# Kernel tuning notes

Hardware: AMD Instinct MI355X
Metric: run time of the kernel (lower is better)

Reference implementation:

```python
import jax, jax.numpy as jnp
import numpy as np

N_NODES = 100000


def _gcn_norm(edge_index, n):
    # add self-loops, then symmetric deg^{-1/2} normalization (PyG GCNConv default)
    loop = jnp.arange(n, dtype=edge_index.dtype)
    src = jnp.concatenate([edge_index[0], loop])
    dst = jnp.concatenate([edge_index[1], loop])
    ones = jnp.ones(src.shape[0], dtype=jnp.float32)
    deg = jax.ops.segment_sum(ones, dst, num_segments=n)
    dinv = jnp.where(deg > 0, jax.lax.rsqrt(deg), 0.0)
    norm = dinv[src] * dinv[dst]  # [E + N]
    return src, dst, norm


def _gcn_conv(x, src, dst, norm, W, b, n):
    h = x @ W                                    # [N, out] transform first (out <= in)
    msg = norm[:, None] * h[src]                 # [E+N, out]
    agg = jax.ops.segment_sum(msg, dst, num_segments=n)
    return agg + b


def reference(x, edge_index, W1, b1, W2, b2):
    n = x.shape[0]
    src, dst, norm = _gcn_norm(edge_index, n)
    h = jax.nn.relu(_gcn_conv(x, src, dst, norm, W1, b1, n))
    # dropout is identity in eval mode (training=False)
    h = jax.nn.relu(_gcn_conv(h, src, dst, norm, W2, b2, n))
    return jax.nn.log_softmax(h, axis=1)


def setup_inputs() -> dict:
    key = jax.random.key(0)
    k1, k2, k3, k4 = jax.random.split(key, 4)
    n, e, f, h, c = N_NODES, 1600000, 500, 64, 40
    x = jax.random.normal(k1, (n, f), dtype=jnp.float32)
    edge_index = jax.random.randint(k2, (2, e), 0, n, dtype=jnp.int64)
    W1 = jax.random.normal(k3, (f, h), dtype=jnp.float32) * (1.0 / np.sqrt(f))
    b1 = jnp.zeros((h,), dtype=jnp.float32)
    W2 = jax.random.normal(k4, (h, c), dtype=jnp.float32) * (1.0 / np.sqrt(h))
    b2 = jnp.zeros((c,), dtype=jnp.float32)
    return {"x": x, "edge_index": edge_index, "W1": W1, "b1": b1, "W2": W2, "b2": b2}
```

## Files before the change

kernel.cpp:

```cpp
#include <hip/hip_runtime.h>

#define NN_F 500
#define HID 64
#define NC 40
#define SCAN_T 256
#define SCAN_E 8
#define SCAN_B (SCAN_T * SCAN_E)
#define LDS_S 40

typedef short s8v __attribute__((ext_vector_type(8)));
typedef short s4v __attribute__((ext_vector_type(4)));
typedef float f4v __attribute__((ext_vector_type(4)));

__device__ __forceinline__ unsigned short rne_bf16(float x) {
    unsigned u = __float_as_uint(x);
    return (unsigned short)((u + 0x7fffu + ((u >> 16) & 1u)) >> 16);
}
__device__ __forceinline__ float bf16_lo(unsigned v) {
    return __uint_as_float(v << 16);
}
__device__ __forceinline__ float bf16_hi(unsigned v) {
    return __uint_as_float(v & 0xffff0000u);
}

__device__ __forceinline__ int load_edge(const void* ei, long long idx, int is64) {
    if (is64) return (int)((const long long*)ei)[idx];
    return ((const int*)ei)[idx];
}

__global__ __launch_bounds__(256) void detect_kernel(const unsigned int* w, int* flag) {
    __shared__ unsigned int red[256];
    unsigned int acc = 0;
    for (int i = threadIdx.x; i < 2048; i += 256) acc |= w[2 * i + 1];
    red[threadIdx.x] = acc;
    __syncthreads();
    for (int s = 128; s > 0; s >>= 1) {
        if (threadIdx.x < s) red[threadIdx.x] |= red[threadIdx.x + s];
        __syncthreads();
    }
    if (threadIdx.x == 0) flag[0] = (red[0] == 0u) ? 1 : 0;
}

__global__ __launch_bounds__(256) void deg_kernel(const void* ei, const int* flag,
                                                  int* deg, int E) {
    int is64 = flag[0];
    long long e = (long long)blockIdx.x * 256 + threadIdx.x;
    if (e < E) {
        int d = load_edge(ei, (long long)E + e, is64);
        atomicAdd(&deg[d], 1);
    }
}

__global__ __launch_bounds__(SCAN_T) void scan1(const int* __restrict__ deg,
                                                int* __restrict__ off,
                                                int* __restrict__ bsums,
                                                float* __restrict__ dinv, int n) {
    __shared__ int lds[SCAN_T];
    int base = blockIdx.x * SCAN_B + threadIdx.x * SCAN_E;
    int v[SCAN_E];
    int local = 0;
#pragma unroll
    for (int k = 0; k < SCAN_E; ++k) {
        int i = base + k;
        v[k] = (i < n) ? deg[i] : 0;
        if (i < n) dinv[i] = rsqrtf((float)v[k] + 1.0f);
        local += v[k];
    }
    lds[threadIdx.x] = local;
    __syncthreads();
    for (int o = 1; o < SCAN_T; o <<= 1) {
        int t = (threadIdx.x >= o) ? lds[threadIdx.x - o] : 0;
        __syncthreads();
        lds[threadIdx.x] += t;
        __syncthreads();
    }
    int prefix = lds[threadIdx.x] - local;
    if (threadIdx.x == SCAN_T - 1) bsums[blockIdx.x] = lds[threadIdx.x];
    int run = prefix;
#pragma unroll
    for (int k = 0; k < SCAN_E; ++k) {
        if (base + k < n) { off[base + k] = run; run += v[k]; }
    }
}

__global__ void scan2(int* bsums, int* off, int nb, int n) {
    int lane = threadIdx.x;
    if (nb <= 64) {
        int v = (lane < nb) ? bsums[lane] : 0;
        int incl = v;
#pragma unroll
        for (int o = 1; o < 64; o <<= 1) {
            int t = __shfl_up(incl, o);
            if (lane >= o) incl += t;
        }
        if (lane < nb) bsums[lane] = incl - v;
        if (lane == 63) off[n] = incl;
    } else if (lane == 0) {
        int run = 0;
        for (int i = 0; i < nb; ++i) { int t = bsums[i]; bsums[i] = run; run += t; }
        off[n] = run;
    }
}

__global__ __launch_bounds__(SCAN_T) void scan3(int* __restrict__ off,
                                                int* __restrict__ cur,
                                                const int* __restrict__ bsums, int n) {
    int base = blockIdx.x * SCAN_B + threadIdx.x * SCAN_E;
    int add = bsums[blockIdx.x];
#pragma unroll
    for (int k = 0; k < SCAN_E; ++k) {
        int i = base + k;
        if (i < n) { int v = off[i] + add; off[i] = v; cur[i] = v; }
    }
}

__global__ __launch_bounds__(256) void build_kernel(const void* ei, const int* flag,
                                                    const float* __restrict__ dinv,
                                                    int* __restrict__ cur,
                                                    int2* __restrict__ csr, int E) {
    int is64 = flag[0];
    long long e = (long long)blockIdx.x * 256 + threadIdx.x;
    if (e >= E) return;
    int s = load_edge(ei, e, is64);
    int d = load_edge(ei, (long long)E + e, is64);
    int pos = atomicAdd(&cur[d], 1);
    csr[pos] = make_int2(s, (int)__float_as_uint(dinv[s] * dinv[d]));
}

__global__ __launch_bounds__(256) void wprep2(const float* __restrict__ W1,
                                              const float* __restrict__ W2,
                                              unsigned short* __restrict__ Wt1,
                                              unsigned short* __restrict__ Wt2) {
    int id = blockIdx.x * 256 + threadIdx.x;
    if (id < 64 * 512) {
        int nn = id >> 9, k = id & 511;
        float v = (k < NN_F) ? W1[k * HID + nn] : 0.f;
        Wt1[id] = rne_bf16(v);
    } else {
        int id2 = id - 64 * 512;
        if (id2 >= 64 * 64) return;
        int nn = id2 >> 6, k = id2 & 63;
        float v = (nn < NC) ? W2[k * NC + nn] : 0.f;
        Wt2[id2] = rne_bf16(v);
    }
}

template<int KPAD>
__global__ __launch_bounds__(256) void gemm_mfma(const float* __restrict__ A,
                                                 const unsigned short* __restrict__ Wh,
                                                 unsigned short* __restrict__ out,
                                                 int n, int K) {
    __shared__ unsigned short Xh[128 * LDS_S];
    __shared__ unsigned short Bh[64 * LDS_S];
    const int t = threadIdx.x;
    const int row0 = blockIdx.x * 128;
    const int wid = t >> 6, lane = t & 63, q = lane >> 4, nn = lane & 15;

    f4v acc[2][4];
#pragma unroll
    for (int mt = 0; mt < 2; ++mt)
#pragma unroll
        for (int ct = 0; ct < 4; ++ct) acc[mt][ct] = (f4v){0.f, 0.f, 0.f, 0.f};

    for (int k0 = 0; k0 < KPAD; k0 += 32) {
        {
            int bn = t >> 2, kq = t & 3;
            *(s8v*)&Bh[bn * LDS_S + kq * 8] = *(const s8v*)&Wh[bn * KPAD + k0 + kq * 8];
        }
        {
            int kq = t & 7, rbase = t >> 3;
#pragma unroll
            for (int rr = 0; rr < 4; ++rr) {
                int row = rr * 32 + rbase;
                int grow = row0 + row;
                int k = k0 + kq * 4;
                float v0 = 0.f, v1 = 0.f, v2 = 0.f, v3 = 0.f;
                if (grow < n) {
                    if (k + 4 <= K) {
                        float4 v = *(const float4*)&A[(long long)grow * K + k];
                        v0 = v.x; v1 = v.y; v2 = v.z; v3 = v.w;
                    } else {
                        if (k + 0 < K) v0 = A[(long long)grow * K + k + 0];
                        if (k + 1 < K) v1 = A[(long long)grow * K + k + 1];
                        if (k + 2 < K) v2 = A[(long long)grow * K + k + 2];
                        if (k + 3 < K) v3 = A[(long long)grow * K + k + 3];
                    }
                }
                s4v h4;
                h4[0] = (short)rne_bf16(v0);
                h4[1] = (short)rne_bf16(v1);
                h4[2] = (short)rne_bf16(v2);
                h4[3] = (short)rne_bf16(v3);
                *(s4v*)&Xh[row * LDS_S + kq * 4] = h4;
            }
        }
        __syncthreads();

        const s8v ah0 = *(const s8v*)&Xh[(wid * 32 + nn) * LDS_S + q * 8];
        const s8v ah1 = *(const s8v*)&Xh[(wid * 32 + 16 + nn) * LDS_S + q * 8];
#pragma unroll
        for (int ct = 0; ct < 4; ++ct) {
            const s8v bh = *(const s8v*)&Bh[(ct * 16 + nn) * LDS_S + q * 8];
            acc[0][ct] = __builtin_amdgcn_mfma_f32_16x16x32_bf16(ah0, bh, acc[0][ct], 0, 0, 0);
            acc[1][ct] = __builtin_amdgcn_mfma_f32_16x16x32_bf16(ah1, bh, acc[1][ct], 0, 0, 0);
        }
        __syncthreads();
    }

#pragma unroll
    for (int mt = 0; mt < 2; ++mt)
#pragma unroll
        for (int ct = 0; ct < 4; ++ct)
#pragma unroll
            for (int r = 0; r < 4; ++r) {
                int row = row0 + wid * 32 + mt * 16 + q * 4 + r;
                if (row < n) out[(long long)row * 64 + ct * 16 + nn] = rne_bf16(acc[mt][ct][r]);
            }
}

#define FMA8(W, H)                                          \
    acc[0] = fmaf(W, bf16_lo((H).x), acc[0]);               \
    acc[1] = fmaf(W, bf16_hi((H).x), acc[1]);               \
    acc[2] = fmaf(W, bf16_lo((H).y), acc[2]);               \
    acc[3] = fmaf(W, bf16_hi((H).y), acc[3]);               \
    acc[4] = fmaf(W, bf16_lo((H).z), acc[4]);               \
    acc[5] = fmaf(W, bf16_hi((H).z), acc[5]);               \
    acc[6] = fmaf(W, bf16_lo((H).w), acc[6]);               \
    acc[7] = fmaf(W, bf16_hi((H).w), acc[7])

__global__ __launch_bounds__(256) void gather_l1(const int2* __restrict__ csr,
                                                 const int* __restrict__ off,
                                                 const unsigned short* __restrict__ h,
                                                 const float* __restrict__ dinv,
                                                 const float* __restrict__ b,
                                                 float* __restrict__ agg, int n) {
    const int lane = threadIdx.x & 63;
    const int g = lane >> 3, fl = lane & 7;
    const int node = __builtin_amdgcn_readfirstlane(blockIdx.x * 4 + (threadIdx.x >> 6));
    if (node >= n) return;
    const int start = off[node], end = off[node + 1];
    float acc[8];
#pragma unroll
    for (int k = 0; k < 8; ++k) acc[k] = 0.f;
    int j = start;
    for (; j + 16 <= end; j += 16) {
        int2 ea = csr[j + g];
        int2 eb = csr[j + 8 + g];
        uint4 ha = *(const uint4*)(h + (long long)ea.x * 64 + fl * 8);
        uint4 hb = *(const uint4*)(h + (long long)eb.x * 64 + fl * 8);
        float wa = __uint_as_float((unsigned)ea.y);
        float wb = __uint_as_float((unsigned)eb.y);
        FMA8(wa, ha);
        FMA8(wb, hb);
    }
    for (; j < end; j += 8) {
        int jj = j + g;
        int2 e = csr[jj < end ? jj : end - 1];
        float w = (jj < end) ? __uint_as_float((unsigned)e.y) : 0.f;
        uint4 hv = *(const uint4*)(h + (long long)e.x * 64 + fl * 8);
        FMA8(w, hv);
    }
#pragma unroll
    for (int k = 0; k < 8; ++k) {
        acc[k] += __shfl_xor(acc[k], 8);
        acc[k] += __shfl_xor(acc[k], 16);
        acc[k] += __shfl_xor(acc[k], 32);
    }
    if (g == 0) {
        float dv = dinv[node];
        float w = dv * dv;
        uint4 hn = *(const uint4*)(h + (long long)node * 64 + fl * 8);
        FMA8(w, hn);
        float4 b4a = ((const float4*)b)[fl * 2];
        float4 b4b = ((const float4*)b)[fl * 2 + 1];
        float4 o0, o1;
        o0.x = acc[0] + b4a.x; o0.x = o0.x > 0.f ? o0.x : 0.f;
        o0.y = acc[1] + b4a.y; o0.y = o0.y > 0.f ? o0.y : 0.f;
        o0.z = acc[2] + b4a.z; o0.z = o0.z > 0.f ? o0.z : 0.f;
        o0.w = acc[3] + b4a.w; o0.w = o0.w > 0.f ? o0.w : 0.f;
        o1.x = acc[4] + b4b.x; o1.x = o1.x > 0.f ? o1.x : 0.f;
        o1.y = acc[5] + b4b.y; o1.y = o1.y > 0.f ? o1.y : 0.f;
        o1.z = acc[6] + b4b.z; o1.z = o1.z > 0.f ? o1.z : 0.f;
        o1.w = acc[7] + b4b.w; o1.w = o1.w > 0.f ? o1.w : 0.f;
        float4* dst = (float4*)(agg + (long long)node * 64 + fl * 8);
        dst[0] = o0;
        dst[1] = o1;
    }
}

__global__ __launch_bounds__(256) void gather_l2(const int2* __restrict__ csr,
                                                 const int* __restrict__ off,
                                                 const unsigned short* __restrict__ h,
                                                 const float* __restrict__ dinv,
                                                 const float* __restrict__ b,
                                                 float* __restrict__ out, int n) {
    const int lane = threadIdx.x & 63;
    const int g = lane >> 3, fl = lane & 7;
    const int node = __builtin_amdgcn_readfirstlane(blockIdx.x * 4 + (threadIdx.x >> 6));
    if (node >= n) return;
    const int start = off[node], end = off[node + 1];
    float acc[8];
#pragma unroll
    for (int k = 0; k < 8; ++k) acc[k] = 0.f;
    int j = start;
    for (; j + 16 <= end; j += 16) {
        int2 ea = csr[j + g];
        int2 eb = csr[j + 8 + g];
        if (fl < 5) {
            uint4 ha = *(const uint4*)(h + (long long)ea.x * 64 + fl * 8);
            uint4 hb = *(const uint4*)(h + (long long)eb.x * 64 + fl * 8);
            float wa = __uint_as_float((unsigned)ea.y);
            float wb = __uint_as_float((unsigned)eb.y);
            FMA8(wa, ha);
            FMA8(wb, hb);
        }
    }
    for (; j < end; j += 8) {
        int jj = j + g;
        int2 e = csr[jj < end ? jj : end - 1];
        if (fl < 5) {
            float w = (jj < end) ? __uint_as_float((unsigned)e.y) : 0.f;
            uint4 hv = *(const uint4*)(h + (long long)e.x * 64 + fl * 8);
            FMA8(w, hv);
        }
    }
#pragma unroll
    for (int k = 0; k < 8; ++k) {
        acc[k] += __shfl_xor(acc[k], 8);
        acc[k] += __shfl_xor(acc[k], 16);
        acc[k] += __shfl_xor(acc[k], 32);
    }
    float v[8];
    float vmax = -1e30f;
    if (fl < 5) {
        float dv = dinv[node];
        float w = dv * dv;
        uint4 hn = *(const uint4*)(h + (long long)node * 64 + fl * 8);
        FMA8(w, hn);
        float4 b4a = ((const float4*)b)[fl * 2];
        float4 b4b = ((const float4*)b)[fl * 2 + 1];
        v[0] = acc[0] + b4a.x; v[1] = acc[1] + b4a.y;
        v[2] = acc[2] + b4a.z; v[3] = acc[3] + b4a.w;
        v[4] = acc[4] + b4b.x; v[5] = acc[5] + b4b.y;
        v[6] = acc[6] + b4b.z; v[7] = acc[7] + b4b.w;
#pragma unroll
        for (int k = 0; k < 8; ++k) {
            v[k] = v[k] > 0.f ? v[k] : 0.f;
            vmax = fmaxf(vmax, v[k]);
        }
    }
#pragma unroll
    for (int o = 1; o < 8; o <<= 1) vmax = fmaxf(vmax, __shfl_xor(vmax, o));
    float ssum = 0.f;
    if (fl < 5) {
#pragma unroll
        for (int k = 0; k < 8; ++k) ssum += expf(v[k] - vmax);
    }
#pragma unroll
    for (int o = 1; o < 8; o <<= 1) ssum += __shfl_xor(ssum, o);
    if (g == 0 && fl < 5) {
        float ls = vmax + logf(ssum);
        float4 o0 = make_float4(v[0] - ls, v[1] - ls, v[2] - ls, v[3] - ls);
        float4 o1 = make_float4(v[4] - ls, v[5] - ls, v[6] - ls, v[7] - ls);
        float4* dst = (float4*)(out + (long long)node * NC + fl * 8);
        dst[0] = o0;
        dst[1] = o1;
    }
}

static inline char* align256(char* p) {
    return (char*)(((uintptr_t)p + 255) & ~(uintptr_t)255);
}

extern "C" void kernel_launch(void* const* d_in, const int* in_sizes, int n_in,
                              void* d_out, int out_size, void* d_ws, size_t ws_size,
                              hipStream_t stream) {
    const float* x  = (const float*)d_in[0];
    const void*  ei = d_in[1];
    const float* W1 = (const float*)d_in[2];
    const float* b1 = (const float*)d_in[3];
    const float* W2 = (const float*)d_in[4];
    const float* b2 = (const float*)d_in[5];
    float* out = (float*)d_out;
    const int n = in_sizes[0] / NN_F;
    const int E = in_sizes[1] / 2;
    const int nScanBlocks = (n + SCAN_B - 1) / SCAN_B;

    char* p = (char*)d_ws;
    int* flag = (int*)p;                 p = align256(p + 16 * sizeof(int));
    int* deg  = (int*)p;                 p = align256(p + (size_t)n * sizeof(int));
    int* off  = (int*)p;                 p = align256(p + (size_t)(n + 1) * sizeof(int));
    int* cur  = (int*)p;                 p = align256(p + (size_t)n * sizeof(int));
    int* bsums = (int*)p;                p = align256(p + 256 * sizeof(int));
    float* dinv = (float*)p;             p = align256(p + (size_t)n * sizeof(float));
    int2* csr = (int2*)p;                p = align256(p + (size_t)E * sizeof(int2));
    unsigned short* Wt1 = (unsigned short*)p; p = align256(p + (size_t)64 * 512 * sizeof(short));
    unsigned short* Wt2 = (unsigned short*)p; p = align256(p + (size_t)64 * 64 * sizeof(short));
    unsigned short* h1 = (unsigned short*)p; p = align256(p + (size_t)n * 64 * sizeof(unsigned short));
    float* agg1 = (float*)p;             p = align256(p + (size_t)n * 64 * sizeof(float));
    unsigned short* h2 = h1;

    (void)hipMemsetAsync(deg, 0, (size_t)n * sizeof(int), stream);
    detect_kernel<<<1, 256, 0, stream>>>((const unsigned int*)ei, flag);
    deg_kernel<<<(E + 255) / 256, 256, 0, stream>>>(ei, flag, deg, E);

    scan1<<<nScanBlocks, SCAN_T, 0, stream>>>(deg, off, bsums, dinv, n);
    scan2<<<1, 64, 0, stream>>>(bsums, off, nScanBlocks, n);
    scan3<<<nScanBlocks, SCAN_T, 0, stream>>>(off, cur, bsums, n);
    build_kernel<<<(E + 255) / 256, 256, 0, stream>>>(ei, flag, dinv, cur, csr, E);

    wprep2<<<(64 * 512 + 64 * 64 + 255) / 256, 256, 0, stream>>>(W1, W2, Wt1, Wt2);

    const int gBlocks = (n + 127) / 128;
    gemm_mfma<512><<<gBlocks, 256, 0, stream>>>(x, Wt1, h1, n, NN_F);
    gather_l1<<<(n + 3) / 4, 256, 0, stream>>>(csr, off, h1, dinv, b1, agg1, n);

    gemm_mfma<64><<<gBlocks, 256, 0, stream>>>(agg1, Wt2, h2, n, HID);
    gather_l2<<<(n + 3) / 4, 256, 0, stream>>>(csr, off, h2, dinv, b2, out, n);
}
```

Baseline: 575.1 us.

## Fuse preprocessing kernels, co-schedule CSR build with GEMM1, store bf16 intermediates

Merges the int64 detection into per-block checks inside the degree and build kernels, folds weight prep into the degree kernel, and replaces scan2+scan3 with a single scan_fin kernel when there are few scan blocks. The CSR build is launched in the same grid as the first GEMM so the atomic scatter overlaps with the compute-bound tiles. Layer-1 aggregation now writes bf16 relu output instead of fp32, and the second GEMM writes a 40-wide h2, cutting bytes for gemm2 and the layer-2 gather. The aim is fewer launches and less memory traffic. The cost is extra rounding on the intermediate and that each block redundantly reads edge words to detect the index width.

After: 549.7 us. 4.4% less time.

```diff
diff --git a/kernel.cpp b/kernel.cpp
--- a/kernel.cpp
+++ b/kernel.cpp
@@ -28,22 +28,39 @@
     return ((const int*)ei)[idx];
 }
 
-__global__ __launch_bounds__(256) void detect_kernel(const unsigned int* w, int* flag) {
-    __shared__ unsigned int red[256];
+__device__ __forceinline__ int detect_is64_block(const void* ei, int E) {
+    const unsigned int* w = (const unsigned int*)ei;
     unsigned int acc = 0;
-    for (int i = threadIdx.x; i < 2048; i += 256) acc |= w[2 * i + 1];
-    red[threadIdx.x] = acc;
+    int i = threadIdx.x;
+    if (i < 256 && i < E) acc = w[2 * i + 1];
+    int any = __any(acc != 0u);
+    __shared__ int red[4];
+    if ((threadIdx.x & 63) == 0) red[threadIdx.x >> 6] = any;
     __syncthreads();
-    for (int s = 128; s > 0; s >>= 1) {
-        if (threadIdx.x < s) red[threadIdx.x] |= red[threadIdx.x + s];
-        __syncthreads();
-    }
-    if (threadIdx.x == 0) flag[0] = (red[0] == 0u) ? 1 : 0;
-}
-
-__global__ __launch_bounds__(256) void deg_kernel(const void* ei, const int* flag,
-                                                  int* deg, int E) {
-    int is64 = flag[0];
+    return (red[0] | red[1] | red[2] | red[3]) == 0;
+}
+
+__global__ __launch_bounds__(256) void deg_wprep(const void* ei, int* __restrict__ deg,
+                                                 const float* __restrict__ W1,
+                                                 const float* __restrict__ W2,
+                                                 unsigned short* __restrict__ Wt1,
+                                                 unsigned short* __restrict__ Wt2,
+                                                 int E, int degBlocks) {
+    if ((int)blockIdx.x >= degBlocks) {
+        int id = ((int)blockIdx.x - degBlocks) * 256 + threadIdx.x;
+        if (id < 64 * 512) {
+            int nn = id >> 9, k = id & 511;
+            Wt1[id] = rne_bf16(k < NN_F ? W1[k * HID + nn] : 0.f);
+        } else {
+            int id2 = id - 64 * 512;
+            if (id2 < 64 * 64) {
+                int nn = id2 >> 6, k = id2 & 63;
+                Wt2[id2] = rne_bf16(nn < NC ? W2[k * NC + nn] : 0.f);
+            }
+        }
+        return;
+    }
+    int is64 = detect_is64_block(ei, E);
     long long e = (long long)blockIdx.x * 256 + threadIdx.x;
     if (e < E) {
         int d = load_edge(ei, (long long)E + e, is64);
@@ -83,25 +100,31 @@
     }
 }
 
+__global__ __launch_bounds__(SCAN_T) void scan_fin(int* __restrict__ off,
+                                                   int* __restrict__ cur,
+                                                   const int* __restrict__ bsums,
+                                                   int n, int nb) {
+    const int lane = threadIdx.x & 63;
+    int v = (lane < nb && lane < (int)blockIdx.x) ? bsums[lane] : 0;
+#pragma unroll
+    for (int o = 1; o < 64; o <<= 1) v += __shfl_xor(v, o);
+    const int add = v;
+    if ((int)blockIdx.x == nb - 1 && threadIdx.x == 0) off[n] = add + bsums[nb - 1];
+    int base = blockIdx.x * SCAN_B + threadIdx.x * SCAN_E;
+#pragma unroll
+    for (int k = 0; k < SCAN_E; ++k) {
+        int i = base + k;
+        if (i < n) { int t = off[i] + add; off[i] = t; cur[i] = t; }
+    }
+}
+
 __global__ void scan2(int* bsums, int* off, int nb, int n) {
-    int lane = threadIdx.x;
-    if (nb <= 64) {
-        int v = (lane < nb) ? bsums[lane] : 0;
-        int incl = v;
-#pragma unroll
-        for (int o = 1; o < 64; o <<= 1) {
-            int t = __shfl_up(incl, o);
-            if (lane >= o) incl += t;
-        }
-        if (lane < nb) bsums[lane] = incl - v;
-        if (lane == 63) off[n] = incl;
-    } else if (lane == 0) {
+    if (threadIdx.x == 0 && blockIdx.x == 0) {
         int run = 0;
         for (int i = 0; i < nb; ++i) { int t = bsums[i]; bsums[i] = run; run += t; }
         off[n] = run;
     }
 }
-
 __global__ __launch_bounds__(SCAN_T) void scan3(int* __restrict__ off,
                                                 int* __restrict__ cur,
                                                 const int* __restrict__ bsums, int n) {
@@ -114,46 +137,14 @@
     }
 }
 
-__global__ __launch_bounds__(256) void build_kernel(const void* ei, const int* flag,
-                                                    const float* __restrict__ dinv,
-                                                    int* __restrict__ cur,
-                                                    int2* __restrict__ csr, int E) {
-    int is64 = flag[0];
-    long long e = (long long)blockIdx.x * 256 + threadIdx.x;
-    if (e >= E) return;
-    int s = load_edge(ei, e, is64);
-    int d = load_edge(ei, (long long)E + e, is64);
-    int pos = atomicAdd(&cur[d], 1);
-    csr[pos] = make_int2(s, (int)__float_as_uint(dinv[s] * dinv[d]));
-}
-
-__global__ __launch_bounds__(256) void wprep2(const float* __restrict__ W1,
-                                              const float* __restrict__ W2,
-                                              unsigned short* __restrict__ Wt1,
-                                              unsigned short* __restrict__ Wt2) {
-    int id = blockIdx.x * 256 + threadIdx.x;
-    if (id < 64 * 512) {
-        int nn = id >> 9, k = id & 511;
-        float v = (k < NN_F) ? W1[k * HID + nn] : 0.f;
-        Wt1[id] = rne_bf16(v);
-    } else {
-        int id2 = id - 64 * 512;
-        if (id2 >= 64 * 64) return;
-        int nn = id2 >> 6, k = id2 & 63;
-        float v = (nn < NC) ? W2[k * NC + nn] : 0.f;
-        Wt2[id2] = rne_bf16(v);
-    }
-}
-
-template<int KPAD>
-__global__ __launch_bounds__(256) void gemm_mfma(const float* __restrict__ A,
-                                                 const unsigned short* __restrict__ Wh,
-                                                 unsigned short* __restrict__ out,
-                                                 int n, int K) {
-    __shared__ unsigned short Xh[128 * LDS_S];
-    __shared__ unsigned short Bh[64 * LDS_S];
+template<int KPAD, bool ABF16, int OUTW>
+__device__ __forceinline__ void gemm_tile(const void* Av,
+                                          const unsigned short* __restrict__ Wh,
+                                          unsigned short* __restrict__ out,
+                                          int n, int K, int bIdx,
+                                          unsigned short* Xh, unsigned short* Bh) {
     const int t = threadIdx.x;
-    const int row0 = blockIdx.x * 128;
+    const int row0 = bIdx * 128;
     const int wid = t >> 6, lane = t & 63, q = lane >> 4, nn = lane & 15;
 
     f4v acc[2][4];
@@ -167,7 +158,19 @@
             int bn = t >> 2, kq = t & 3;
             *(s8v*)&Bh[bn * LDS_S + kq * 8] = *(const s8v*)&Wh[bn * KPAD + k0 + kq * 8];
         }
-        {
+        if (ABF16) {
+            const unsigned short* A = (const unsigned short*)Av;
+            int kq = t & 3, rbase = t >> 2;
+#pragma unroll
+            for (int rr = 0; rr < 2; ++rr) {
+                int row = rr * 64 + rbase;
+                int grow = row0 + row;
+                s8v h8 = (s8v){0, 0, 0, 0, 0, 0, 0, 0};
+                if (grow < n) h8 = *(const s8v*)&A[(long long)grow * KPAD + k0 + kq * 8];
+                *(s8v*)&Xh[row * LDS_S + kq * 8] = h8;
+            }
+        } else {
+            const float* A = (const float*)Av;
             int kq = t & 7, rbase = t >> 3;
 #pragma unroll
             for (int rr = 0; rr < 4; ++rr) {
@@ -210,12 +213,48 @@
 #pragma unroll
     for (int mt = 0; mt < 2; ++mt)
 #pragma unroll
-        for (int ct = 0; ct < 4; ++ct)
-#pragma unroll
-            for (int r = 0; r < 4; ++r) {
-                int row = row0 + wid * 32 + mt * 16 + q * 4 + r;
-                if (row < n) out[(long long)row * 64 + ct * 16 + nn] = rne_bf16(acc[mt][ct][r]);
+        for (int ct = 0; ct < 4; ++ct) {
+            int col = ct * 16 + nn;
+            if (col < OUTW) {
+#pragma unroll
+                for (int r = 0; r < 4; ++r) {
+                    int row = row0 + wid * 32 + mt * 16 + q * 4 + r;
+                    if (row < n) out[(long long)row * OUTW + col] = rne_bf16(acc[mt][ct][r]);
+                }
             }
+        }
+}
+
+__global__ __launch_bounds__(256) void build_gemm1(const void* ei,
+                                                   const float* __restrict__ dinv,
+                                                   int* __restrict__ cur,
+                                                   int2* __restrict__ csr, int E,
+                                                   int gemmBlocks,
+                                                   const float* __restrict__ x,
+                                                   const unsigned short* __restrict__ Wt1,
+                                                   unsigned short* __restrict__ h1, int n) {
+    __shared__ unsigned short Xh[128 * LDS_S];
+    __shared__ unsigned short Bh[64 * LDS_S];
+    if ((int)blockIdx.x < gemmBlocks) {
+        gemm_tile<512, false, 64>(x, Wt1, h1, n, NN_F, blockIdx.x, Xh, Bh);
+        return;
+    }
+    int b = (int)blockIdx.x - gemmBlocks;
+    int is64 = detect_is64_block(ei, E);
+    long long e = (long long)b * 256 + threadIdx.x;
+    if (e >= E) return;
+    int s = load_edge(ei, e, is64);
+    int d = load_edge(ei, (long long)E + e, is64);
+    int pos = atomicAdd(&cur[d], 1);
+    csr[pos] = make_int2(s, (int)__float_as_uint(dinv[s] * dinv[d]));
+}
+
+__global__ __launch_bounds__(256) void gemm2_kernel(const unsigned short* __restrict__ relu1,
+                                                    const unsigned short* __restrict__ Wt2,
+                                                    unsigned short* __restrict__ h2, int n) {
+    __shared__ unsigned short Xh[128 * LDS_S];
+    __shared__ unsigned short Bh[64 * LDS_S];
+    gemm_tile<64, true, 40>(relu1, Wt2, h2, n, HID, blockIdx.x, Xh, Bh);
 }
 
 #define FMA8(W, H)                                          \
@@ -233,7 +272,7 @@
                                                  const unsigned short* __restrict__ h,
                                                  const float* __restrict__ dinv,
                                                  const float* __restrict__ b,
-                                                 float* __restrict__ agg, int n) {
+                                                 unsigned short* __restrict__ relu1, int n) {
     const int lane = threadIdx.x & 63;
     const int g = lane >> 3, fl = lane & 7;
     const int node = __builtin_amdgcn_readfirstlane(blockIdx.x * 4 + (threadIdx.x >> 6));
@@ -273,18 +312,16 @@
         FMA8(w, hn);
         float4 b4a = ((const float4*)b)[fl * 2];
         float4 b4b = ((const float4*)b)[fl * 2 + 1];
-        float4 o0, o1;
-        o0.x = acc[0] + b4a.x; o0.x = o0.x > 0.f ? o0.x : 0.f;
-        o0.y = acc[1] + b4a.y; o0.y = o0.y > 0.f ? o0.y : 0.f;
-        o0.z = acc[2] + b4a.z; o0.z = o0.z > 0.f ? o0.z : 0.f;
-        o0.w = acc[3] + b4a.w; o0.w = o0.w > 0.f ? o0.w : 0.f;
-        o1.x = acc[4] + b4b.x; o1.x = o1.x > 0.f ? o1.x : 0.f;
-        o1.y = acc[5] + b4b.y; o1.y = o1.y > 0.f ? o1.y : 0.f;
-        o1.z = acc[6] + b4b.z; o1.z = o1.z > 0.f ? o1.z : 0.f;
-        o1.w = acc[7] + b4b.w; o1.w = o1.w > 0.f ? o1.w : 0.f;
-        float4* dst = (float4*)(agg + (long long)node * 64 + fl * 8);
-        dst[0] = o0;
-        dst[1] = o1;
+        float o[8];
+        o[0] = acc[0] + b4a.x; o[1] = acc[1] + b4a.y;
+        o[2] = acc[2] + b4a.z; o[3] = acc[3] + b4a.w;
+        o[4] = acc[4] + b4b.x; o[5] = acc[5] + b4b.y;
+        o[6] = acc[6] + b4b.z; o[7] = acc[7] + b4b.w;
+        s8v r;
+#pragma unroll
+        for (int k = 0; k < 8; ++k)
+            r[k] = (short)rne_bf16(o[k] > 0.f ? o[k] : 0.f);
+        *(s8v*)&relu1[(long long)node * 64 + fl * 8] = r;
     }
 }
 
@@ -307,8 +344,8 @@
         int2 ea = csr[j + g];
         int2 eb = csr[j + 8 + g];
         if (fl < 5) {
-            uint4 ha = *(const uint4*)(h + (long long)ea.x * 64 + fl * 8);
-            uint4 hb = *(const uint4*)(h + (long long)eb.x * 64 + fl * 8);
+            uint4 ha = *(const uint4*)(h + (long long)ea.x * 40 + fl * 8);
+            uint4 hb = *(const uint4*)(h + (long long)eb.x * 40 + fl * 8);
             float wa = __uint_as_float((unsigned)ea.y);
             float wb = __uint_as_float((unsigned)eb.y);
             FMA8(wa, ha);
@@ -320,7 +357,7 @@
         int2 e = csr[jj < end ? jj : end - 1];
         if (fl < 5) {
             float w = (jj < end) ? __uint_as_float((unsigned)e.y) : 0.f;
-            uint4 hv = *(const uint4*)(h + (long long)e.x * 64 + fl * 8);
+            uint4 hv = *(const uint4*)(h + (long long)e.x * 40 + fl * 8);
             FMA8(w, hv);
         }
     }
@@ -335,7 +372,7 @@
     if (fl < 5) {
         float dv = dinv[node];
         float w = dv * dv;
-        uint4 hn = *(const uint4*)(h + (long long)node * 64 + fl * 8);
+        uint4 hn = *(const uint4*)(h + (long long)node * 40 + fl * 8);
         FMA8(w, hn);
         float4 b4a = ((const float4*)b)[fl * 2];
         float4 b4b = ((const float4*)b)[fl * 2 + 1];
@@ -385,9 +422,10 @@
     const int n = in_sizes[0] / NN_F;
     const int E = in_sizes[1] / 2;
     const int nScanBlocks = (n + SCAN_B - 1) / SCAN_B;
+    const int degBlocks = (E + 255) / 256;
+    const int gemmBlocks = (n + 127) / 128;
 
     char* p = (char*)d_ws;
-    int* flag = (int*)p;                 p = align256(p + 16 * sizeof(int));
     int* deg  = (int*)p;                 p = align256(p + (size_t)n * sizeof(int));
     int* off  = (int*)p;                 p = align256(p + (size_t)(n + 1) * sizeof(int));
     int* cur  = (int*)p;                 p = align256(p + (size_t)n * sizeof(int));
@@ -397,24 +435,24 @@
     unsigned short* Wt1 = (unsigned short*)p; p = align256(p + (size_t)64 * 512 * sizeof(short));
     unsigned short* Wt2 = (unsigned short*)p; p = align256(p + (size_t)64 * 64 * sizeof(short));
     unsigned short* h1 = (unsigned short*)p; p = align256(p + (size_t)n * 64 * sizeof(unsigned short));
-    float* agg1 = (float*)p;             p = align256(p + (size_t)n * 64 * sizeof(float));
+    unsigned short* relu1 = (unsigned short*)p; p = align256(p + (size_t)n * 64 * sizeof(unsigned short));
     unsigned short* h2 = h1;
 
     (void)hipMemsetAsync(deg, 0, (size_t)n * sizeof(int), stream);
-    detect_kernel<<<1, 256, 0, stream>>>((const unsigned int*)ei, flag);
-    deg_kernel<<<(E + 255) / 256, 256, 0, stream>>>(ei, flag, deg, E);
+    deg_wprep<<<degBlocks + 144, 256, 0, stream>>>(ei, deg, W1, W2, Wt1, Wt2, E, degBlocks);
 
     scan1<<<nScanBlocks, SCAN_T, 0, stream>>>(deg, off, bsums, dinv, n);
-    scan2<<<1, 64, 0, stream>>>(bsums, off, nScanBlocks, n);
-    scan3<<<nScanBlocks, SCAN_T, 0, stream>>>(off, cur, bsums, n);
-    build_kernel<<<(E + 255) / 256, 256, 0, stream>>>(ei, flag, dinv, cur, csr, E);
-
-    wprep2<<<(64 * 512 + 64 * 64 + 255) / 256, 256, 0, stream>>>(W1, W2, Wt1, Wt2);
-
-    const int gBlocks = (n + 127) / 128;
-    gemm_mfma<512><<<gBlocks, 256, 0, stream>>>(x, Wt1, h1, n, NN_F);
-    gather_l1<<<(n + 3) / 4, 256, 0, stream>>>(csr, off, h1, dinv, b1, agg1, n);
-
-    gemm_mfma<64><<<gBlocks, 256, 0, stream>>>(agg1, Wt2, h2, n, HID);
+    if (nScanBlocks <= 64) {
+        scan_fin<<<nScanBlocks, SCAN_T, 0, stream>>>(off, cur, bsums, n, nScanBlocks);
+    } else {
+        scan2<<<1, 64, 0, stream>>>(bsums, off, nScanBlocks, n);
+        scan3<<<nScanBlocks, SCAN_T, 0, stream>>>(off, cur, bsums, n);
+    }
+
+    build_gemm1<<<gemmBlocks + degBlocks, 256, 0, stream>>>(ei, dinv, cur, csr, E,
+                                                            gemmBlocks, x, Wt1, h1, n);
+
+    gather_l1<<<(n + 3) / 4, 256, 0, stream>>>(csr, off, h1, dinv, b1, relu1, n);
+    gemm2_kernel<<<gemmBlocks, 256, 0, stream>>>(relu1, Wt2, h2, n);
     gather_l2<<<(n + 3) / 4, 256, 0, stream>>>(csr, off, h2, dinv, b2, out, n);
 }
```
